# Kernel tuning notes

Hardware: AMD Instinct MI355X
Metric: run time of the kernel (lower is better)

Reference implementation:

```python
import jax, jax.numpy as jnp
import numpy as np

N_NODES = 50000
K = 16            # fixed node degree (regular graph -> reshapeable edge list)
N_FEAT = 128
N_TEMPL = 16
M_TEMPL = 8
ALPHA = 0.5       # FGW structure/feature trade-off


def setup_inputs() -> dict:
    key = jax.random.key(0)
    k1, k2, k3, k4 = jax.random.split(key, 4)
    x = jax.random.normal(k1, (N_NODES, N_FEAT), dtype=jnp.float32)
    # fixed-degree graph: node i has exactly K neighbors -> edge_index[1] reshapes to [N, K]
    dst = jax.random.randint(k2, (N_NODES * K,), 0, N_NODES)
    src = jnp.repeat(jnp.arange(N_NODES), K)
    edge_index = jnp.stack([src, dst])  # [2, N*K]
    templates = jax.random.uniform(k3, (N_TEMPL, M_TEMPL, M_TEMPL), dtype=jnp.float32)
    templates_features = jax.random.uniform(k4, (N_TEMPL, M_TEMPL, N_FEAT), dtype=jnp.float32)
    return {"x": x, "edge_index": edge_index,
            "templates": templates, "templates_features": templates_features}


def reference(x, edge_index, templates, templates_features):
    """LTFWG forward: per-node FGW distance between the node's 1-hop induced
    subgraph (neighbor features + induced adjacency) and each learned template,
    evaluated under the uniform product coupling (closed form). Output [N, T]."""
    n = x.shape[0]
    nbrs = edge_index[1].reshape(n, K)               # [N,K] neighbor ids per node
    f = x[nbrs]                                      # [N,K,F] gathered neighbor features

    # ---- feature (Wasserstein) term: E_a||f_a||^2 + E_c||Ft_c||^2 - 2<E_a f_a, E_c Ft_c>
    sq = jnp.mean(jnp.sum(f * f, axis=-1), axis=-1)                 # [N]
    fmean = jnp.mean(f, axis=1)                                     # [N,F]
    tsq = jnp.mean(jnp.sum(templates_features ** 2, axis=-1), -1)   # [T]
    tmean = jnp.mean(templates_features, axis=1)                    # [T,F]
    feat = sq[:, None] + tsq[None, :] - 2.0 * (fmean @ tmean.T)     # [N,T]

    # ---- structure (Gromov) term with induced adjacency among the K neighbors
    non = nbrs[nbrs]                                  # [N,K,K] neighbors-of-neighbors
    # C[n,a,b] = 1 iff nbrs[n,b] is a neighbor of nbrs[n,a]
    C = jnp.any(non[:, :, :, None] == nbrs[:, None, None, :], axis=2).astype(x.dtype)
    mC = jnp.mean(C, axis=(1, 2))                     # [N]; C binary -> mean(C^2)=mean(C)
    mCt = jnp.mean(templates, axis=(1, 2))            # [T]
    mCt2 = jnp.mean(templates ** 2, axis=(1, 2))      # [T]
    struct = mC[:, None] + mCt2[None, :] - 2.0 * mC[:, None] * mCt[None, :]  # [N,T]

    return (1.0 - ALPHA) * feat + ALPHA * struct
```

## Files before the change

### kernel.cpp

```cpp
#include <hip/hip_runtime.h>
#include <stdint.h>

#define N_NODES 50000
#define KDEG    16
#define NFEAT   128
#define NTPL    16
#define MTPL    8
#define NTILES  ((N_NODES + 63) / 64)

#define TMEAN_OFF 0
#define TSQ_OFF   2048
#define MCT_OFF   2064
#define MCT2_OFF  2080
#define Z_OFF     2112
#define WS_FLOATS (Z_OFF + N_NODES * NTPL)
#define WS_BYTES  ((size_t)WS_FLOATS * 4)

__global__ __launch_bounds__(256, 4)
void ltfwg_zbuild(const float* __restrict__ x,
                  const float* __restrict__ tmpl,
                  const float* __restrict__ tfeat,
                  float* __restrict__ ws) {
    const int tid = threadIdx.x;

    __shared__ float tm_lds[NTPL * 144];

    {
        const int f  = tid & 127;
        const int t0 = (tid >> 7) * 8;
        #pragma unroll
        for (int k = 0; k < 8; ++k) {
            int t = t0 + k;
            float s = 0.f;
            #pragma unroll
            for (int m = 0; m < MTPL; ++m)
                s += tfeat[t * (MTPL * NFEAT) + m * NFEAT + f];
            tm_lds[t * 144 + (f >> 5) * 36 + (f & 31)] = s * 0.125f;
        }
    }

    if (blockIdx.x == 0) {
        const int t = tid >> 4;
        const int j = tid & 15;
        float ssq = 0.f;
        #pragma unroll
        for (int m = 0; m < MTPL; ++m)
            #pragma unroll
            for (int c = 0; c < 8; ++c) {
                float v = tfeat[t * (MTPL * NFEAT) + m * NFEAT + j * 8 + c];
                ssq += v * v;
            }
        float sv = 0.f, sv2 = 0.f;
        #pragma unroll
        for (int c = 0; c < 4; ++c) {
            float v = tmpl[t * 64 + j * 4 + c];
            sv += v;
            sv2 += v * v;
        }
        #pragma unroll
        for (int off = 1; off <= 8; off <<= 1) {
            ssq += __shfl_xor(ssq, off);
            sv  += __shfl_xor(sv, off);
            sv2 += __shfl_xor(sv2, off);
        }
        if (j == 0) {
            ws[TSQ_OFF + t]  = ssq * 0.125f;
            ws[MCT_OFF + t]  = sv  * (1.f / 64.f);
            ws[MCT2_OFF + t] = sv2 * (1.f / 64.f);
        }
    }
    __syncthreads();

    const int q  = tid & 3;
    const int rr = tid >> 2;
    for (int tile = blockIdx.x; tile < NTILES; tile += gridDim.x) {
        int n = tile * 64 + rr;
        if (n < N_NODES) {
            const float4* x4 = (const float4*)x + (size_t)n * 32 + q * 8;
            float4 xv[8];
            #pragma unroll
            for (int jj = 0; jj < 8; ++jj) xv[jj] = x4[jj];

            float s2 = 0.f;
            #pragma unroll
            for (int jj = 0; jj < 8; ++jj)
                s2 += xv[jj].x * xv[jj].x + xv[jj].y * xv[jj].y +
                      xv[jj].z * xv[jj].z + xv[jj].w * xv[jj].w;

            float acc[NTPL];
            #pragma unroll
            for (int t = 0; t < NTPL; ++t) {
                const float* tb = tm_lds + t * 144 + q * 36;
                float a = 0.f;
                #pragma unroll
                for (int jj = 0; jj < 8; ++jj) {
                    float4 tv = *(const float4*)(tb + 4 * jj);
                    a += xv[jj].x * tv.x + xv[jj].y * tv.y +
                         xv[jj].z * tv.z + xv[jj].w * tv.w;
                }
                acc[t] = a;
            }

            float h = s2;
            h += __shfl_xor(h, 1);
            h += __shfl_xor(h, 2);
            h *= 0.5f;
            #pragma unroll
            for (int t = 0; t < NTPL; ++t) {
                acc[t] += __shfl_xor(acc[t], 1);
                acc[t] += __shfl_xor(acc[t], 2);
            }
            float b0, b1, b2, b3;
            if (q == 0)      { b0 = acc[0];  b1 = acc[1];  b2 = acc[2];  b3 = acc[3];  }
            else if (q == 1) { b0 = acc[4];  b1 = acc[5];  b2 = acc[6];  b3 = acc[7];  }
            else if (q == 2) { b0 = acc[8];  b1 = acc[9];  b2 = acc[10]; b3 = acc[11]; }
            else             { b0 = acc[12]; b1 = acc[13]; b2 = acc[14]; b3 = acc[15]; }
            float4 zz = make_float4(h - b0, h - b1, h - b2, h - b3);
            ((float4*)(ws + Z_OFF))[(size_t)n * 4 + q] = zz;
        }
    }
}

__global__ __launch_bounds__(256, 8)
void ltfwg_gather(const int* __restrict__ dst, const float* __restrict__ ws,
                  float* __restrict__ out) {
    const int lane   = threadIdx.x & 63;
    const int gwave  = (blockIdx.x * blockDim.x + threadIdx.x) >> 6;
    const int nwaves = (gridDim.x * blockDim.x) >> 6;
    const int a = lane & 15;
    const int c = lane >> 4;

    const int tl = c * 4 + (lane & 3);
    const float A  = 0.5f * (ws[TSQ_OFF + tl] + ws[MCT2_OFF + tl]);
    const float Bc = 0.5f - ws[MCT_OFF + tl];
    const bool writer = (lane & 15) < 4;
    const float4* z4 = (const float4*)(ws + Z_OFF);
    const int4*  d4 = (const int4*)dst;

    int n = gwave;
    int nbr = (n < N_NODES) ? dst[n * KDEG + a] : 0;
    while (n < N_NODES) {
        const int n2 = n + nwaves;
        int nbr_next = (n2 < N_NODES) ? dst[n2 * KDEG + a] : 0;

        float4 v  = z4[(size_t)nbr * 4 + c];
        int4   cv = d4[(size_t)nbr * 4 + c];

        uint32_t m = 0;
        #pragma unroll
        for (int b = 0; b < KDEG; ++b) {
            int vb = __builtin_amdgcn_readlane(nbr, b);
            uint32_t hit = (uint32_t)((cv.x == vb) | (cv.y == vb) |
                                      (cv.z == vb) | (cv.w == vb));
            m |= hit << b;
        }
        m |= (uint32_t)__shfl_xor((int)m, 16);
        m |= (uint32_t)__shfl_xor((int)m, 32);
        int cm = __popc(m);
        cm += __shfl_xor(cm, 1);
        cm += __shfl_xor(cm, 2);
        cm += __shfl_xor(cm, 4);
        cm += __shfl_xor(cm, 8);

        float v0 = v.x, v1 = v.y, v2 = v.z, v3 = v.w;
        #pragma unroll
        for (int off = 1; off <= 8; off <<= 1) {
            v0 += __shfl_xor(v0, off);
            v1 += __shfl_xor(v1, off);
            v2 += __shfl_xor(v2, off);
            v3 += __shfl_xor(v3, off);
        }

        if (writer) {
            int j = lane & 3;
            float dsel = (j == 0) ? v0 : (j == 1) ? v1 : (j == 2) ? v2 : v3;
            float val = 0.0625f * dsel + A + (float)cm * (1.f / 256.f) * Bc;
            out[n * NTPL + tl] = val;
        }
        n = n2;
        nbr = nbr_next;
    }
}

__global__ void ltfwg_prep(const float* __restrict__ tmpl,
                           const float* __restrict__ tfeat,
                           float* __restrict__ ws) {
    const int t   = blockIdx.x;
    const int tid = threadIdx.x;
    float s = 0.f, ssq = 0.f;
    #pragma unroll
    for (int m = 0; m < MTPL; ++m) {
        float v = tfeat[t * (MTPL * NFEAT) + m * NFEAT + tid];
        s += v;
        ssq += v * v;
    }
    ws[TMEAN_OFF + t * NFEAT + tid] = s * 0.125f;
    __shared__ float red[128];
    red[tid] = ssq;
    __syncthreads();
    for (int o = 64; o > 0; o >>= 1) {
        if (tid < o) red[tid] += red[tid + o];
        __syncthreads();
    }
    if (tid == 0) ws[TSQ_OFF + t] = red[0] * 0.125f;
    if (tid < 64) {
        float v = tmpl[t * 64 + tid];
        float sv = v, sv2 = v * v;
        #pragma unroll
        for (int off = 32; off >= 1; off >>= 1) {
            sv  += __shfl_xor(sv, off);
            sv2 += __shfl_xor(sv2, off);
        }
        if (tid == 0) {
            ws[MCT_OFF + t]  = sv  * (1.f / 64.f);
            ws[MCT2_OFF + t] = sv2 * (1.f / 64.f);
        }
    }
}

__global__ __launch_bounds__(256, 4)
void ltfwg_fallback(const float* __restrict__ x, const int* __restrict__ dst,
                    const float* __restrict__ ws, float* __restrict__ out) {
    const int lane   = threadIdx.x & 63;
    const int wave   = (blockIdx.x * blockDim.x + threadIdx.x) >> 6;
    const int nwaves = (gridDim.x * blockDim.x) >> 6;
    float tm0[NTPL], tm1[NTPL];
    #pragma unroll
    for (int t = 0; t < NTPL; ++t) {
        float2 tv = ((const float2*)(ws + TMEAN_OFF + t * NFEAT))[lane];
        tm0[t] = tv.x;
        tm1[t] = tv.y;
    }
    const int tl = lane & 15;
    const float A  = 0.5f * (ws[TSQ_OFF + tl] + ws[MCT2_OFF + tl]);
    const float Bc = 0.5f - ws[MCT_OFF + tl];
    for (int n = wave; n < N_NODES; n += nwaves) {
        const int nbr = dst[n * KDEG + (lane & 15)];
        float fs0 = 0.f, fs1 = 0.f, sqa = 0.f;
        #pragma unroll
        for (int a = 0; a < KDEG; ++a) {
            int nid = __shfl(nbr, a);
            float2 fv = ((const float2*)x)[nid * (NFEAT / 2) + lane];
            fs0 += fv.x; fs1 += fv.y;
            sqa += fv.x * fv.x + fv.y * fv.y;
        }
        float dotp[NTPL];
        #pragma unroll
        for (int t = 0; t < NTPL; ++t) dotp[t] = fs0 * tm0[t] + fs1 * tm1[t];
        int nida = __shfl(nbr, lane >> 2);
        int4 cv = ((const int4*)(dst + nida * KDEG))[lane & 3];
        uint32_t m = 0;
        #pragma unroll
        for (int b = 0; b < KDEG; ++b) {
            int vb = __shfl(nbr, b);
            uint32_t hit = (uint32_t)((cv.x == vb) | (cv.y == vb) |
                                      (cv.z == vb) | (cv.w == vb));
            m |= hit << b;
        }
        m |= (uint32_t)__shfl_xor((int)m, 1);
        m |= (uint32_t)__shfl_xor((int)m, 2);
        float cnt = (float)__popc(m);
        #pragma unroll
        for (int off = 32; off >= 1; off >>= 1) {
            sqa += __shfl_xor(sqa, off);
            cnt += __shfl_xor(cnt, off);
            #pragma unroll
            for (int t = 0; t < NTPL; ++t) dotp[t] += __shfl_xor(dotp[t], off);
        }
        float dsel = dotp[0];
        #pragma unroll
        for (int t = 1; t < NTPL; ++t) dsel = (lane == t) ? dotp[t] : dsel;
        if (lane < NTPL) {
            float mC = cnt * (1.0f / 1024.0f);
            out[n * NTPL + lane] = 0.03125f * sqa - 0.0625f * dsel + A + mC * Bc;
        }
    }
}

extern "C" void kernel_launch(void* const* d_in, const int* in_sizes, int n_in,
                              void* d_out, int out_size, void* d_ws, size_t ws_size,
                              hipStream_t stream) {
    const float* x     = (const float*)d_in[0];
    const int*   edge  = (const int*)d_in[1];
    const float* tmpl  = (const float*)d_in[2];
    const float* tfeat = (const float*)d_in[3];
    float* ws  = (float*)d_ws;
    float* out = (float*)d_out;
    const int* dst = edge + (N_NODES * KDEG);

    if (ws_size >= WS_BYTES) {
        ltfwg_zbuild<<<NTILES, 256, 0, stream>>>(x, tmpl, tfeat, ws);
        ltfwg_gather<<<2048, 256, 0, stream>>>(dst, ws, out);
    } else {
        ltfwg_prep<<<NTPL, 128, 0, stream>>>(tmpl, tfeat, ws);
        ltfwg_fallback<<<1024, 256, 0, stream>>>(x, dst, ws, out);
    }
}
```

Before: 104.7 us.

## Process two nodes per thread in zbuild and use DPP row reductions

The z-building kernel now has each thread handle two nodes per tile (128 nodes per block). Each template-mean value loaded from shared memory is reused for two dot products, which halves the number of blocks and LDS reads. Cross-lane reductions in both kernels switch from __shfl_xor to DPP row-rotate and quad-permute adds, which skip the LDS-based shuffle path. In exchange, register pressure rises (launch bounds drop from 4 to 3 blocks), and the DPP rotate-within-row sums must match the old xor-butterfly semantics.

```diff
diff --git a/kernel.cpp b/kernel.cpp
--- a/kernel.cpp
+++ b/kernel.cpp
@@ -6,7 +6,7 @@
 #define NFEAT   128
 #define NTPL    16
 #define MTPL    8
-#define NTILES  ((N_NODES + 63) / 64)
+#define NTILES2 ((N_NODES + 127) / 128)
 
 #define TMEAN_OFF 0
 #define TSQ_OFF   2048
@@ -16,7 +16,44 @@
 #define WS_FLOATS (Z_OFF + N_NODES * NTPL)
 #define WS_BYTES  ((size_t)WS_FLOATS * 4)
 
-__global__ __launch_bounds__(256, 4)
+template<int CTRL>
+__device__ __forceinline__ float dpp_addf(float v) {
+    int t = __builtin_amdgcn_update_dpp(0, __float_as_int(v), CTRL, 0xF, 0xF, 1);
+    return v + __int_as_float(t);
+}
+template<int CTRL>
+__device__ __forceinline__ int dpp_addi(int v) {
+    int t = __builtin_amdgcn_update_dpp(0, v, CTRL, 0xF, 0xF, 1);
+    return v + t;
+}
+#define ROR1 0x121
+#define ROR2 0x122
+#define ROR4 0x124
+#define ROR8 0x128
+#define QPX1 0xB1
+#define QPX2 0x4E
+
+__device__ __forceinline__ float row16_sum(float v) {
+    v = dpp_addf<ROR1>(v);
+    v = dpp_addf<ROR2>(v);
+    v = dpp_addf<ROR4>(v);
+    v = dpp_addf<ROR8>(v);
+    return v;
+}
+__device__ __forceinline__ int row16_sumi(int v) {
+    v = dpp_addi<ROR1>(v);
+    v = dpp_addi<ROR2>(v);
+    v = dpp_addi<ROR4>(v);
+    v = dpp_addi<ROR8>(v);
+    return v;
+}
+__device__ __forceinline__ float quad_sum(float v) {
+    v = dpp_addf<QPX1>(v);
+    v = dpp_addf<QPX2>(v);
+    return v;
+}
+
+__global__ __launch_bounds__(256, 3)
 void ltfwg_zbuild(const float* __restrict__ x,
                   const float* __restrict__ tmpl,
                   const float* __restrict__ tfeat,
@@ -57,12 +94,9 @@
             sv += v;
             sv2 += v * v;
         }
-        #pragma unroll
-        for (int off = 1; off <= 8; off <<= 1) {
-            ssq += __shfl_xor(ssq, off);
-            sv  += __shfl_xor(sv, off);
-            sv2 += __shfl_xor(sv2, off);
-        }
+        ssq = row16_sum(ssq);
+        sv  = row16_sum(sv);
+        sv2 = row16_sum(sv2);
         if (j == 0) {
             ws[TSQ_OFF + t]  = ssq * 0.125f;
             ws[MCT_OFF + t]  = sv  * (1.f / 64.f);
@@ -73,51 +107,73 @@
 
     const int q  = tid & 3;
     const int rr = tid >> 2;
-    for (int tile = blockIdx.x; tile < NTILES; tile += gridDim.x) {
-        int n = tile * 64 + rr;
-        if (n < N_NODES) {
-            const float4* x4 = (const float4*)x + (size_t)n * 32 + q * 8;
-            float4 xv[8];
-            #pragma unroll
-            for (int jj = 0; jj < 8; ++jj) xv[jj] = x4[jj];
-
-            float s2 = 0.f;
-            #pragma unroll
-            for (int jj = 0; jj < 8; ++jj)
-                s2 += xv[jj].x * xv[jj].x + xv[jj].y * xv[jj].y +
-                      xv[jj].z * xv[jj].z + xv[jj].w * xv[jj].w;
-
-            float acc[NTPL];
-            #pragma unroll
-            for (int t = 0; t < NTPL; ++t) {
-                const float* tb = tm_lds + t * 144 + q * 36;
-                float a = 0.f;
-                #pragma unroll
-                for (int jj = 0; jj < 8; ++jj) {
-                    float4 tv = *(const float4*)(tb + 4 * jj);
-                    a += xv[jj].x * tv.x + xv[jj].y * tv.y +
-                         xv[jj].z * tv.z + xv[jj].w * tv.w;
-                }
-                acc[t] = a;
+    for (int tile = blockIdx.x; tile < NTILES2; tile += gridDim.x) {
+        const int n0 = tile * 128 + rr;
+        const int n1 = n0 + 64;
+        const bool ok0 = (n0 < N_NODES), ok1 = (n1 < N_NODES);
+
+        float4 xa[8], xb[8];
+        if (ok0) {
+            const float4* x4 = (const float4*)x + (size_t)n0 * 32 + q * 8;
+            #pragma unroll
+            for (int jj = 0; jj < 8; ++jj) xa[jj] = x4[jj];
+        }
+        if (ok1) {
+            const float4* x4 = (const float4*)x + (size_t)n1 * 32 + q * 8;
+            #pragma unroll
+            for (int jj = 0; jj < 8; ++jj) xb[jj] = x4[jj];
+        }
+        if (!ok0) break;
+
+        float s2a = 0.f, s2b = 0.f;
+        #pragma unroll
+        for (int jj = 0; jj < 8; ++jj) {
+            s2a += xa[jj].x * xa[jj].x + xa[jj].y * xa[jj].y +
+                   xa[jj].z * xa[jj].z + xa[jj].w * xa[jj].w;
+            if (ok1)
+                s2b += xb[jj].x * xb[jj].x + xb[jj].y * xb[jj].y +
+                       xb[jj].z * xb[jj].z + xb[jj].w * xb[jj].w;
+        }
+
+        float acc0[NTPL], acc1[NTPL];
+        #pragma unroll
+        for (int t = 0; t < NTPL; ++t) {
+            const float* tb = tm_lds + t * 144 + q * 36;
+            float a0 = 0.f, a1 = 0.f;
+            #pragma unroll
+            for (int jj = 0; jj < 8; ++jj) {
+                float4 tv = *(const float4*)(tb + 4 * jj);
+                a0 += xa[jj].x * tv.x + xa[jj].y * tv.y +
+                      xa[jj].z * tv.z + xa[jj].w * tv.w;
+                a1 += xb[jj].x * tv.x + xb[jj].y * tv.y +
+                      xb[jj].z * tv.z + xb[jj].w * tv.w;
             }
-
-            float h = s2;
-            h += __shfl_xor(h, 1);
-            h += __shfl_xor(h, 2);
-            h *= 0.5f;
-            #pragma unroll
-            for (int t = 0; t < NTPL; ++t) {
-                acc[t] += __shfl_xor(acc[t], 1);
-                acc[t] += __shfl_xor(acc[t], 2);
-            }
-            float b0, b1, b2, b3;
-            if (q == 0)      { b0 = acc[0];  b1 = acc[1];  b2 = acc[2];  b3 = acc[3];  }
-            else if (q == 1) { b0 = acc[4];  b1 = acc[5];  b2 = acc[6];  b3 = acc[7];  }
-            else if (q == 2) { b0 = acc[8];  b1 = acc[9];  b2 = acc[10]; b3 = acc[11]; }
-            else             { b0 = acc[12]; b1 = acc[13]; b2 = acc[14]; b3 = acc[15]; }
-            float4 zz = make_float4(h - b0, h - b1, h - b2, h - b3);
-            ((float4*)(ws + Z_OFF))[(size_t)n * 4 + q] = zz;
-        }
+            acc0[t] = a0;
+            acc1[t] = a1;
+        }
+
+        float h0 = quad_sum(s2a) * 0.5f;
+        float h1 = quad_sum(s2b) * 0.5f;
+        #pragma unroll
+        for (int t = 0; t < NTPL; ++t) {
+            acc0[t] = quad_sum(acc0[t]);
+            acc1[t] = quad_sum(acc1[t]);
+        }
+
+        float a0, a1, a2, a3, b0, b1, b2, b3;
+        if (q == 0)      { a0=acc0[0];  a1=acc0[1];  a2=acc0[2];  a3=acc0[3];
+                           b0=acc1[0];  b1=acc1[1];  b2=acc1[2];  b3=acc1[3];  }
+        else if (q == 1) { a0=acc0[4];  a1=acc0[5];  a2=acc0[6];  a3=acc0[7];
+                           b0=acc1[4];  b1=acc1[5];  b2=acc1[6];  b3=acc1[7];  }
+        else if (q == 2) { a0=acc0[8];  a1=acc0[9];  a2=acc0[10]; a3=acc0[11];
+                           b0=acc1[8];  b1=acc1[9];  b2=acc1[10]; b3=acc1[11]; }
+        else             { a0=acc0[12]; a1=acc0[13]; a2=acc0[14]; a3=acc0[15];
+                           b0=acc1[12]; b1=acc1[13]; b2=acc1[14]; b3=acc1[15]; }
+        ((float4*)(ws + Z_OFF))[(size_t)n0 * 4 + q] =
+            make_float4(h0 - a0, h0 - a1, h0 - a2, h0 - a3);
+        if (ok1)
+            ((float4*)(ws + Z_OFF))[(size_t)n1 * 4 + q] =
+                make_float4(h1 - b0, h1 - b1, h1 - b2, h1 - b3);
     }
 }
 
@@ -156,20 +212,12 @@
         }
         m |= (uint32_t)__shfl_xor((int)m, 16);
         m |= (uint32_t)__shfl_xor((int)m, 32);
-        int cm = __popc(m);
-        cm += __shfl_xor(cm, 1);
-        cm += __shfl_xor(cm, 2);
-        cm += __shfl_xor(cm, 4);
-        cm += __shfl_xor(cm, 8);
-
-        float v0 = v.x, v1 = v.y, v2 = v.z, v3 = v.w;
-        #pragma unroll
-        for (int off = 1; off <= 8; off <<= 1) {
-            v0 += __shfl_xor(v0, off);
-            v1 += __shfl_xor(v1, off);
-            v2 += __shfl_xor(v2, off);
-            v3 += __shfl_xor(v3, off);
-        }
+        int cm = row16_sumi(__popc(m));
+
+        float v0 = row16_sum(v.x);
+        float v1 = row16_sum(v.y);
+        float v2 = row16_sum(v.z);
+        float v3 = row16_sum(v.w);
 
         if (writer) {
             int j = lane & 3;
@@ -238,8 +286,8 @@
         const int nbr = dst[n * KDEG + (lane & 15)];
         float fs0 = 0.f, fs1 = 0.f, sqa = 0.f;
         #pragma unroll
-        for (int a = 0; a < KDEG; ++a) {
-            int nid = __shfl(nbr, a);
+        for (int aa = 0; aa < KDEG; ++aa) {
+            int nid = __shfl(nbr, aa);
             float2 fv = ((const float2*)x)[nid * (NFEAT / 2) + lane];
             fs0 += fv.x; fs1 += fv.y;
             sqa += fv.x * fv.x + fv.y * fv.y;
@@ -289,7 +337,7 @@
     const int* dst = edge + (N_NODES * KDEG);
 
     if (ws_size >= WS_BYTES) {
-        ltfwg_zbuild<<<NTILES, 256, 0, stream>>>(x, tmpl, tfeat, ws);
+        ltfwg_zbuild<<<NTILES2, 256, 0, stream>>>(x, tmpl, tfeat, ws);
         ltfwg_gather<<<2048, 256, 0, stream>>>(dst, ws, out);
     } else {
         ltfwg_prep<<<NTPL, 128, 0, stream>>>(tmpl, tfeat, ws);
```

Measured after the change: 158.3 us. +51.2%, slower.
